# Kernel optimization log

Hardware: AMD Instinct MI355X
Metric: run time of the kernel (lower is better)

Reference implementation:

```python
import jax, jax.numpy as jnp
import numpy as np

DIM = 320
NUM_HEADS = 5
HEAD_DIM = DIM // NUM_HEADS  # 64
SCALE = HEAD_DIM ** -0.5


def setup_inputs() -> dict:
    key = jax.random.key(0)
    k1, k2, k3, k4 = jax.random.split(key, 4)
    B, N, C = 8, 2048, DIM
    x = jax.random.normal(k1, (B, N, C), dtype=jnp.float32)
    # nn.Linear(dim, dim*3, bias=False): weight [3*dim, dim]
    w_qkv = jax.random.normal(k2, (3 * C, C), dtype=jnp.float32) * (C ** -0.5)
    # nn.Linear(dim, dim): weight [dim, dim], bias [dim]
    w_proj = jax.random.normal(k3, (C, C), dtype=jnp.float32) * (C ** -0.5)
    b_proj = jax.random.normal(k4, (C,), dtype=jnp.float32) * 0.01
    return {"x": x, "w_qkv": w_qkv, "w_proj": w_proj, "b_proj": b_proj}


def reference(x, w_qkv, w_proj, b_proj):
    B, N, C = x.shape
    H, D = NUM_HEADS, HEAD_DIM
    # qkv projection: [B, N, 3C] -> [3, B, H, N, D]
    qkv = jnp.einsum('bnc,kc->bnk', x, w_qkv)
    qkv = qkv.reshape(B, N, 3, H, D).transpose(2, 0, 3, 1, 4)
    q, k, v = qkv[0], qkv[1], qkv[2]
    # full attention matrix [B, H, N, N] (retained by original module)
    attn = jnp.einsum('bhnd,bhmd->bhnm', q, k) * SCALE
    attn = jax.nn.softmax(attn, axis=-1)
    # attn_drop p=0 -> identity (eval/deterministic)
    out = jnp.einsum('bhnm,bhmd->bhnd', attn, v)
    out = out.transpose(0, 2, 1, 3).reshape(B, N, C)
    out = jnp.einsum('bnc,oc->bno', out, w_proj) + b_proj
    # proj_drop p=0 -> identity
    return out
```

## Files before the change

### kernel.cpp

```cpp
#include <hip/hip_runtime.h>
#include <hip/hip_bf16.h>


typedef __attribute__((ext_vector_type(8))) short bf16x8;
typedef __attribute__((ext_vector_type(4))) float f32x4;

#define MFMA(a, b, c) __builtin_amdgcn_mfma_f32_16x16x32_bf16((a), (b), (c), 0, 0, 0)

#define QSCALE 0.18033688322643216f

static __device__ inline bf16x8 ld8(const __hip_bfloat16* p) {
    return *reinterpret_cast<const bf16x8*>(p);
}

static __device__ inline unsigned short bfbits(float v) {
    unsigned int u = __builtin_bit_cast(unsigned int, v);
    u += 0x7FFFu + ((u >> 16) & 1u);
    return (unsigned short)(u >> 16);
}

static __device__ inline bf16x8 cvt8(const float* src) {
    float4 a = *reinterpret_cast<const float4*>(src);
    float4 b = *reinterpret_cast<const float4*>(src + 4);
    bf16x8 v;
    v[0] = (short)bfbits(a.x); v[1] = (short)bfbits(a.y);
    v[2] = (short)bfbits(a.z); v[3] = (short)bfbits(a.w);
    v[4] = (short)bfbits(b.x); v[5] = (short)bfbits(b.y);
    v[6] = (short)bfbits(b.z); v[7] = (short)bfbits(b.w);
    return v;
}

__global__ __launch_bounds__(256)
void cvt_x(const float* __restrict__ x, __hip_bfloat16* __restrict__ xb)
{
    const size_t tid = (size_t)blockIdx.x * blockDim.x + threadIdx.x;
    const size_t stride = (size_t)gridDim.x * blockDim.x;
    const float4* x4 = (const float4*)x;
    ushort4* xb4 = (ushort4*)xb;
    for (size_t i = tid; i < 1310720u; i += stride) {
        float4 v = x4[i];
        ushort4 u;
        u.x = bfbits(v.x); u.y = bfbits(v.y);
        u.z = bfbits(v.z); u.w = bfbits(v.w);
        xb4[i] = u;
    }
}

__global__ __launch_bounds__(256)
void qkv_kernel(const __hip_bfloat16* __restrict__ xb,
                const float* __restrict__ w,
                __hip_bfloat16* __restrict__ qout,
                __hip_bfloat16* __restrict__ kp,
                __hip_bfloat16* __restrict__ vp)
{
    __shared__ __align__(16) __hip_bfloat16 As[128 * 72];
    __shared__ __align__(16) __hip_bfloat16 Bs[64 * 72];

    const int tid  = threadIdx.x;
    const int wv   = tid >> 6;
    const int lane = tid & 63;
    const int quad = lane >> 4;
    const int col  = lane & 15;
    const int m0   = blockIdx.x * 128;
    const int n0   = blockIdx.y * 64;

    f32x4 acc[2][4];
#pragma unroll
    for (int i = 0; i < 2; ++i)
#pragma unroll
        for (int j = 0; j < 4; ++j) acc[i][j] = (f32x4){0.f, 0.f, 0.f, 0.f};

    for (int k0 = 0; k0 < 320; k0 += 64) {
        __syncthreads();
#pragma unroll
        for (int i = 0; i < 4; ++i) {
            int ch = tid + i * 256;
            int r = ch >> 3, sg = ch & 7;
            *reinterpret_cast<float4*>(&As[r * 72 + sg * 8]) =
                *reinterpret_cast<const float4*>(&xb[(m0 + r) * 320 + k0 + sg * 8]);
        }
#pragma unroll
        for (int i = 0; i < 2; ++i) {
            int ch = tid + i * 256;
            int r = ch >> 3, sg = ch & 7;
            *reinterpret_cast<bf16x8*>(&Bs[r * 72 + sg * 8]) =
                cvt8(&w[(n0 + r) * 320 + k0 + sg * 8]);
        }
        __syncthreads();

#pragma unroll
        for (int hf = 0; hf < 2; ++hf) {
            bf16x8 a0 = ld8(&As[(wv * 32 + col) * 72 + hf * 32 + quad * 8]);
            bf16x8 a1 = ld8(&As[(wv * 32 + 16 + col) * 72 + hf * 32 + quad * 8]);
#pragma unroll
            for (int nt = 0; nt < 4; ++nt) {
                bf16x8 b = ld8(&Bs[(nt * 16 + col) * 72 + hf * 32 + quad * 8]);
                acc[0][nt] = MFMA(a0, b, acc[0][nt]);
                acc[1][nt] = MFMA(a1, b, acc[1][nt]);
            }
        }
    }

    const int s = blockIdx.y / 5;
    const int h = blockIdx.y % 5;
    unsigned short* qo = (unsigned short*)qout;
    unsigned short* ko = (unsigned short*)kp;
    unsigned short* vo = (unsigned short*)vp;
#pragma unroll
    for (int mt = 0; mt < 2; ++mt) {
#pragma unroll
        for (int nt = 0; nt < 4; ++nt) {
#pragma unroll
            for (int r = 0; r < 4; ++r) {
                int m = m0 + wv * 32 + mt * 16 + quad * 4 + r;
                int d = nt * 16 + col;
                int b = m >> 11, n = m & 2047;
                int bh = b * 5 + h;
                float val = acc[mt][nt][r];
                if (s == 0) {
                    qo[((size_t)bh * 2048 + n) * 64 + d] = bfbits(val * QSCALE);
                } else if (s == 1) {
                    int p = n >> 6, nn = n & 63;
                    size_t a = ((size_t)(bh * 32 + p) * 8 + (d >> 5) * 4 + (nn >> 4)) * 512
                             + (((d >> 3) & 3) * 16 + (nn & 15)) * 8 + (d & 7);
                    ko[a] = bfbits(val);
                } else {
                    int p = n >> 6;
                    size_t a = ((size_t)(bh * 32 + p) * 8 + ((n >> 5) & 1) * 4 + (d >> 4)) * 512
                             + (((n >> 3) & 3) * 16 + (d & 15)) * 8 + (n & 7);
                    vo[a] = bfbits(val);
                }
            }
        }
    }
}

__global__ __launch_bounds__(128)
void attn_kernel(const __hip_bfloat16* __restrict__ Q,
                 const __hip_bfloat16* __restrict__ Kp,
                 const __hip_bfloat16* __restrict__ Vp,
                 __hip_bfloat16* __restrict__ A2)
{
    __shared__ __align__(16) unsigned char smraw[9216];

    const int tid  = threadIdx.x;
    const int wv   = tid >> 6;
    const int lane = tid & 63;
    const int quad = lane >> 4;
    const int col  = lane & 15;
    const int bh = blockIdx.y, b = bh / 5, h = bh % 5;
    const int q0 = blockIdx.x * 32;
    const int t0 = wv * 16;

    __hip_bfloat16* Ps = (__hip_bfloat16*)smraw + wv * 2304;
    unsigned short* ps_w = (unsigned short*)(Ps + (quad * 4) * 72 + col);
    const __hip_bfloat16* ps_r = Ps + col * 72 + quad * 8;

    const __hip_bfloat16* kt = Kp + (size_t)bh * 131072 + (size_t)t0 * 4096 + lane * 8;
    const __hip_bfloat16* vt = Vp + (size_t)bh * 131072 + (size_t)t0 * 4096 + lane * 8;
    const __hip_bfloat16* Qh = Q + (size_t)bh * 131072;

    bf16x8 qf[2][2];
#pragma unroll
    for (int mt = 0; mt < 2; ++mt)
#pragma unroll
        for (int hf = 0; hf < 2; ++hf)
            qf[mt][hf] = ld8(&Qh[(q0 + mt * 16 + col) * 64 + hf * 32 + quad * 8]);

    f32x4 lp[2];
    f32x4 o[2][4];
#pragma unroll
    for (int mt = 0; mt < 2; ++mt) {
        lp[mt] = (f32x4){0.f, 0.f, 0.f, 0.f};
#pragma unroll
        for (int dt = 0; dt < 4; ++dt) o[mt][dt] = (f32x4){0.f, 0.f, 0.f, 0.f};
    }

    bf16x8 ka[8];
#pragma unroll
    for (int f = 0; f < 8; ++f) ka[f] = ld8(kt + f * 512);
    kt += 4096;

    for (int t = 0; t < 16; ++t) {
        f32x4 s[2][4];
#pragma unroll
        for (int mt = 0; mt < 2; ++mt)
#pragma unroll
            for (int nt = 0; nt < 4; ++nt) {
                f32x4 z = (f32x4){0.f, 0.f, 0.f, 0.f};
                z = MFMA(qf[mt][0], ka[nt], z);
                z = MFMA(qf[mt][1], ka[4 + nt], z);
                s[mt][nt] = z;
            }

        bf16x8 va[8];
#pragma unroll
        for (int f = 0; f < 8; ++f) va[f] = ld8(vt + f * 512);
        vt += 4096;

#pragma unroll
        for (int f = 0; f < 8; ++f) ka[f] = ld8(kt + f * 512);
        kt += 4096;

#pragma unroll
        for (int mt = 0; mt < 2; ++mt)
#pragma unroll
            for (int nt = 0; nt < 4; ++nt) {
                f32x4 pv;
#pragma unroll
                for (int r = 0; r < 4; ++r)
                    pv[r] = __builtin_amdgcn_exp2f(s[mt][nt][r]);
                lp[mt] += pv;
#pragma unroll
                for (int r = 0; r < 4; ++r)
                    ps_w[(mt * 16 + r) * 72 + nt * 16] = bfbits(pv[r]);
            }
        __asm__ volatile("s_waitcnt lgkmcnt(0)" ::: "memory");

#pragma unroll
        for (int mt = 0; mt < 2; ++mt)
#pragma unroll
            for (int kk = 0; kk < 2; ++kk) {
                bf16x8 pf = ld8(ps_r + mt * 1152 + kk * 32);
#pragma unroll
                for (int dt = 0; dt < 4; ++dt)
                    o[mt][dt] = MFMA(pf, va[kk * 4 + dt], o[mt][dt]);
            }
    }

    float lval[2][4];
#pragma unroll
    for (int mt = 0; mt < 2; ++mt)
#pragma unroll
        for (int r = 0; r < 4; ++r) {
            float v = lp[mt][r];
#pragma unroll
            for (int off = 1; off < 16; off <<= 1)
                v += __shfl_xor(v, off, 64);
            lval[mt][r] = v;
        }

    float* cbo = (float*)smraw;
    float* cbl = cbo + 2048;
    __syncthreads();
    if (wv == 1) {
#pragma unroll
        for (int mt = 0; mt < 2; ++mt)
#pragma unroll
            for (int dt = 0; dt < 4; ++dt)
#pragma unroll
                for (int r = 0; r < 4; ++r)
                    cbo[(mt * 16 + quad * 4 + r) * 64 + dt * 16 + col] = o[mt][dt][r];
        if (col == 0)
#pragma unroll
            for (int mt = 0; mt < 2; ++mt)
#pragma unroll
                for (int r = 0; r < 4; ++r)
                    cbl[mt * 16 + quad * 4 + r] = lval[mt][r];
    }
    __syncthreads();
    if (wv == 0) {
        unsigned short* a2o = (unsigned short*)A2;
#pragma unroll
        for (int mt = 0; mt < 2; ++mt) {
#pragma unroll
            for (int r = 0; r < 4; ++r) {
                int row = mt * 16 + quad * 4 + r;
                float inv = 1.0f / (lval[mt][r] + cbl[row]);
                int grow = q0 + row;
#pragma unroll
                for (int dt = 0; dt < 4; ++dt) {
                    int d = dt * 16 + col;
                    float val = (o[mt][dt][r] + cbo[row * 64 + d]) * inv;
                    a2o[((size_t)(b * 2048 + grow)) * 320 + h * 64 + d] = bfbits(val);
                }
            }
        }
    }
}

__global__ __launch_bounds__(256)
void proj_kernel(const __hip_bfloat16* __restrict__ a2,
                 const float* __restrict__ w,
                 const float* __restrict__ bias,
                 float* __restrict__ out)
{
    __shared__ __align__(16) __hip_bfloat16 As[128 * 72];
    __shared__ __align__(16) __hip_bfloat16 Bs[64 * 72];

    const int tid  = threadIdx.x;
    const int wv   = tid >> 6;
    const int lane = tid & 63;
    const int quad = lane >> 4;
    const int col  = lane & 15;
    const int m0   = blockIdx.x * 128;
    const int n0   = blockIdx.y * 64;

    f32x4 acc[2][4];
#pragma unroll
    for (int i = 0; i < 2; ++i)
#pragma unroll
        for (int j = 0; j < 4; ++j) acc[i][j] = (f32x4){0.f, 0.f, 0.f, 0.f};

    for (int k0 = 0; k0 < 320; k0 += 64) {
        __syncthreads();
#pragma unroll
        for (int i = 0; i < 4; ++i) {
            int ch = tid + i * 256;
            int r = ch >> 3, sg = ch & 7;
            *reinterpret_cast<float4*>(&As[r * 72 + sg * 8]) =
                *reinterpret_cast<const float4*>(&a2[(m0 + r) * 320 + k0 + sg * 8]);
        }
#pragma unroll
        for (int i = 0; i < 2; ++i) {
            int ch = tid + i * 256;
            int r = ch >> 3, sg = ch & 7;
            *reinterpret_cast<bf16x8*>(&Bs[r * 72 + sg * 8]) =
                cvt8(&w[(n0 + r) * 320 + k0 + sg * 8]);
        }
        __syncthreads();

#pragma unroll
        for (int hf = 0; hf < 2; ++hf) {
            bf16x8 a0 = ld8(&As[(wv * 32 + col) * 72 + hf * 32 + quad * 8]);
            bf16x8 a1 = ld8(&As[(wv * 32 + 16 + col) * 72 + hf * 32 + quad * 8]);
#pragma unroll
            for (int nt = 0; nt < 4; ++nt) {
                bf16x8 b = ld8(&Bs[(nt * 16 + col) * 72 + hf * 32 + quad * 8]);
                acc[0][nt] = MFMA(a0, b, acc[0][nt]);
                acc[1][nt] = MFMA(a1, b, acc[1][nt]);
            }
        }
    }

#pragma unroll
    for (int nt = 0; nt < 4; ++nt) {
        float bv = bias[n0 + nt * 16 + col];
#pragma unroll
        for (int mt = 0; mt < 2; ++mt) {
#pragma unroll
            for (int r = 0; r < 4; ++r) {
                int m = m0 + wv * 32 + mt * 16 + quad * 4 + r;
                out[(size_t)m * 320 + n0 + nt * 16 + col] = acc[mt][nt][r] + bv;
            }
        }
    }
}

extern "C" void kernel_launch(void* const* d_in, const int* in_sizes, int n_in,
                              void* d_out, int out_size, void* d_ws, size_t ws_size,
                              hipStream_t stream)
{
    const float* x      = (const float*)d_in[0];
    const float* w_qkv  = (const float*)d_in[1];
    const float* w_proj = (const float*)d_in[2];
    const float* b_proj = (const float*)d_in[3];
    float* out = (float*)d_out;

    const size_t NX = 5242880;
    __hip_bfloat16* xb = (__hip_bfloat16*)d_ws;
    __hip_bfloat16* q  = xb + NX;
    __hip_bfloat16* kp = q + NX;
    __hip_bfloat16* vp = kp + NX;
    __hip_bfloat16* a2 = xb;

    cvt_x<<<1024, 256, 0, stream>>>(x, xb);
    qkv_kernel<<<dim3(128, 15), 256, 0, stream>>>(xb, w_qkv, q, kp, vp);
    attn_kernel<<<dim3(64, 40), 128, 0, stream>>>(q, kp, vp, a2);
    proj_kernel<<<dim3(128, 5), 256, 0, stream>>>(a2, w_proj, b_proj, out);
}
```

Measured before the change: 187.5 us.

## Compute transposed scores so P feeds PV MFMA from registers, skipping LDS

The QK^T MFMA operands are swapped so each lane holds the score tile transposed. The exponentiated probabilities can then be packed directly into a bf16x4 B operand for the 16x16x16 MFMA, which removes the per-tile LDS write/read round trip and its wait. V is stored in a new 4-element-granular packed layout to match. The epilogue, row-sum reduction and final combine are adjusted for the transposed output accumulator. In exchange it uses twice as many smaller MFMAs and narrower 8-byte V loads.

```diff
diff --git a/kernel.cpp b/kernel.cpp
--- a/kernel.cpp
+++ b/kernel.cpp
@@ -3,9 +3,11 @@
 
 
 typedef __attribute__((ext_vector_type(8))) short bf16x8;
+typedef __attribute__((ext_vector_type(4))) short bf16x4;
 typedef __attribute__((ext_vector_type(4))) float f32x4;
 
-#define MFMA(a, b, c) __builtin_amdgcn_mfma_f32_16x16x32_bf16((a), (b), (c), 0, 0, 0)
+#define MFMA(a, b, c)   __builtin_amdgcn_mfma_f32_16x16x32_bf16((a), (b), (c), 0, 0, 0)
+#define MFMA16(a, b, c) __builtin_amdgcn_mfma_f32_16x16x16bf16_1k((a), (b), (c), 0, 0, 0)
 
 #define QSCALE 0.18033688322643216f
 
@@ -125,9 +127,9 @@
                              + (((d >> 3) & 3) * 16 + (nn & 15)) * 8 + (d & 7);
                     ko[a] = bfbits(val);
                 } else {
-                    int p = n >> 6;
-                    size_t a = ((size_t)(bh * 32 + p) * 8 + ((n >> 5) & 1) * 4 + (d >> 4)) * 512
-                             + (((n >> 3) & 3) * 16 + (d & 15)) * 8 + (n & 7);
+                    int p = n >> 6, n6 = n & 63;
+                    size_t a = ((size_t)(bh * 32 + p) * 16 + (n6 >> 4) * 4 + (d >> 4)) * 256
+                             + (((n6 >> 2) & 3) * 16 + (d & 15)) * 4 + (n6 & 3);
                     vo[a] = bfbits(val);
                 }
             }
@@ -141,7 +143,7 @@
                  const __hip_bfloat16* __restrict__ Vp,
                  __hip_bfloat16* __restrict__ A2)
 {
-    __shared__ __align__(16) unsigned char smraw[9216];
+    __shared__ __align__(16) unsigned char smraw[8448];
 
     const int tid  = threadIdx.x;
     const int wv   = tid >> 6;
@@ -152,12 +154,8 @@
     const int q0 = blockIdx.x * 32;
     const int t0 = wv * 16;
 
-    __hip_bfloat16* Ps = (__hip_bfloat16*)smraw + wv * 2304;
-    unsigned short* ps_w = (unsigned short*)(Ps + (quad * 4) * 72 + col);
-    const __hip_bfloat16* ps_r = Ps + col * 72 + quad * 8;
-
     const __hip_bfloat16* kt = Kp + (size_t)bh * 131072 + (size_t)t0 * 4096 + lane * 8;
-    const __hip_bfloat16* vt = Vp + (size_t)bh * 131072 + (size_t)t0 * 4096 + lane * 8;
+    const __hip_bfloat16* vt = Vp + (size_t)bh * 131072 + (size_t)t0 * 4096 + lane * 4;
     const __hip_bfloat16* Qh = Q + (size_t)bh * 131072;
 
     bf16x8 qf[2][2];
@@ -167,14 +165,14 @@
         for (int hf = 0; hf < 2; ++hf)
             qf[mt][hf] = ld8(&Qh[(q0 + mt * 16 + col) * 64 + hf * 32 + quad * 8]);
 
-    f32x4 lp[2];
-    f32x4 o[2][4];
-#pragma unroll
-    for (int mt = 0; mt < 2; ++mt) {
-        lp[mt] = (f32x4){0.f, 0.f, 0.f, 0.f};
-#pragma unroll
-        for (int dt = 0; dt < 4; ++dt) o[mt][dt] = (f32x4){0.f, 0.f, 0.f, 0.f};
-    }
+    f32x4 lpv[2];
+    f32x4 o[4][2];
+#pragma unroll
+    for (int mt = 0; mt < 2; ++mt) lpv[mt] = (f32x4){0.f, 0.f, 0.f, 0.f};
+#pragma unroll
+    for (int dt = 0; dt < 4; ++dt)
+#pragma unroll
+        for (int mt = 0; mt < 2; ++mt) o[dt][mt] = (f32x4){0.f, 0.f, 0.f, 0.f};
 
     bf16x8 ka[8];
 #pragma unroll
@@ -182,20 +180,21 @@
     kt += 4096;
 
     for (int t = 0; t < 16; ++t) {
-        f32x4 s[2][4];
-#pragma unroll
-        for (int mt = 0; mt < 2; ++mt)
-#pragma unroll
-            for (int nt = 0; nt < 4; ++nt) {
+        f32x4 s[4][2];
+#pragma unroll
+        for (int nt = 0; nt < 4; ++nt)
+#pragma unroll
+            for (int mt = 0; mt < 2; ++mt) {
                 f32x4 z = (f32x4){0.f, 0.f, 0.f, 0.f};
-                z = MFMA(qf[mt][0], ka[nt], z);
-                z = MFMA(qf[mt][1], ka[4 + nt], z);
-                s[mt][nt] = z;
-            }
-
-        bf16x8 va[8];
-#pragma unroll
-        for (int f = 0; f < 8; ++f) va[f] = ld8(vt + f * 512);
+                z = MFMA(ka[nt], qf[mt][0], z);
+                z = MFMA(ka[4 + nt], qf[mt][1], z);
+                s[nt][mt] = z;
+            }
+
+        bf16x4 va[16];
+#pragma unroll
+        for (int f = 0; f < 16; ++f)
+            va[f] = *reinterpret_cast<const bf16x4*>(vt + f * 256);
         vt += 4096;
 
 #pragma unroll
@@ -203,78 +202,63 @@
         kt += 4096;
 
 #pragma unroll
-        for (int mt = 0; mt < 2; ++mt)
-#pragma unroll
-            for (int nt = 0; nt < 4; ++nt) {
+        for (int nt = 0; nt < 4; ++nt) {
+#pragma unroll
+            for (int mt = 0; mt < 2; ++mt) {
                 f32x4 pv;
 #pragma unroll
                 for (int r = 0; r < 4; ++r)
-                    pv[r] = __builtin_amdgcn_exp2f(s[mt][nt][r]);
-                lp[mt] += pv;
-#pragma unroll
-                for (int r = 0; r < 4; ++r)
-                    ps_w[(mt * 16 + r) * 72 + nt * 16] = bfbits(pv[r]);
-            }
-        __asm__ volatile("s_waitcnt lgkmcnt(0)" ::: "memory");
-
-#pragma unroll
-        for (int mt = 0; mt < 2; ++mt)
-#pragma unroll
-            for (int kk = 0; kk < 2; ++kk) {
-                bf16x8 pf = ld8(ps_r + mt * 1152 + kk * 32);
+                    pv[r] = __builtin_amdgcn_exp2f(s[nt][mt][r]);
+                lpv[mt] += pv;
+                bf16x4 pb;
+#pragma unroll
+                for (int r = 0; r < 4; ++r) pb[r] = (short)bfbits(pv[r]);
 #pragma unroll
                 for (int dt = 0; dt < 4; ++dt)
-                    o[mt][dt] = MFMA(pf, va[kk * 4 + dt], o[mt][dt]);
-            }
-    }
-
-    float lval[2][4];
-#pragma unroll
-    for (int mt = 0; mt < 2; ++mt)
-#pragma unroll
-        for (int r = 0; r < 4; ++r) {
-            float v = lp[mt][r];
-#pragma unroll
-            for (int off = 1; off < 16; off <<= 1)
-                v += __shfl_xor(v, off, 64);
-            lval[mt][r] = v;
-        }
+                    o[dt][mt] = MFMA16(va[nt * 4 + dt], pb, o[dt][mt]);
+            }
+        }
+    }
+
+    float lsum[2];
+#pragma unroll
+    for (int mt = 0; mt < 2; ++mt) {
+        float v = lpv[mt][0] + lpv[mt][1] + lpv[mt][2] + lpv[mt][3];
+        v += __shfl_xor(v, 16, 64);
+        v += __shfl_xor(v, 32, 64);
+        lsum[mt] = v;
+    }
 
     float* cbo = (float*)smraw;
     float* cbl = cbo + 2048;
     __syncthreads();
     if (wv == 1) {
 #pragma unroll
-        for (int mt = 0; mt < 2; ++mt)
-#pragma unroll
-            for (int dt = 0; dt < 4; ++dt)
+        for (int dt = 0; dt < 4; ++dt)
+#pragma unroll
+            for (int mt = 0; mt < 2; ++mt)
 #pragma unroll
                 for (int r = 0; r < 4; ++r)
-                    cbo[(mt * 16 + quad * 4 + r) * 64 + dt * 16 + col] = o[mt][dt][r];
-        if (col == 0)
-#pragma unroll
-            for (int mt = 0; mt < 2; ++mt)
-#pragma unroll
-                for (int r = 0; r < 4; ++r)
-                    cbl[mt * 16 + quad * 4 + r] = lval[mt][r];
+                    cbo[(dt * 16 + quad * 4 + r) * 32 + mt * 16 + col] = o[dt][mt][r];
+        if (quad == 0)
+#pragma unroll
+            for (int mt = 0; mt < 2; ++mt) cbl[mt * 16 + col] = lsum[mt];
     }
     __syncthreads();
     if (wv == 0) {
         unsigned short* a2o = (unsigned short*)A2;
 #pragma unroll
         for (int mt = 0; mt < 2; ++mt) {
-#pragma unroll
-            for (int r = 0; r < 4; ++r) {
-                int row = mt * 16 + quad * 4 + r;
-                float inv = 1.0f / (lval[mt][r] + cbl[row]);
-                int grow = q0 + row;
-#pragma unroll
-                for (int dt = 0; dt < 4; ++dt) {
-                    int d = dt * 16 + col;
-                    float val = (o[mt][dt][r] + cbo[row * 64 + d]) * inv;
-                    a2o[((size_t)(b * 2048 + grow)) * 320 + h * 64 + d] = bfbits(val);
+            float inv = 1.0f / (lsum[mt] + cbl[mt * 16 + col]);
+            size_t rowbase = ((size_t)(b * 2048 + q0 + mt * 16 + col)) * 320 + h * 64;
+#pragma unroll
+            for (int dt = 0; dt < 4; ++dt)
+#pragma unroll
+                for (int r = 0; r < 4; ++r) {
+                    int d = dt * 16 + quad * 4 + r;
+                    float val = (o[dt][mt][r] + cbo[d * 32 + mt * 16 + col]) * inv;
+                    a2o[rowbase + d] = bfbits(val);
                 }
-            }
         }
     }
 }
```

New measurement: 190.1 us. No clear change (+1.4%).

## Pre-convert weights to bf16 and compute Q,K,V per head in one block

Applied to the files above, without the earlier changes.

Weight conversion to bf16 moves into the existing x-conversion kernel, so the GEMM kernels load bf16 weights directly instead of converting fp32 on every tile load. The QKV GEMM now has each block compute the Q, K and V outputs for one head, reusing the shared x tile across all three. This cuts the grid from 15 to 5 column blocks and reduces redundant x reads. The cost is 3x the accumulator registers (96 floats) and a larger shared memory footprint, which may reduce occupancy. The grid also shrinks to 640 blocks, which may underfill the GPU.

```diff
diff --git a/kernel.cpp b/kernel.cpp
--- a/kernel.cpp
+++ b/kernel.cpp
@@ -19,24 +19,20 @@
     return (unsigned short)(u >> 16);
 }
 
-static __device__ inline bf16x8 cvt8(const float* src) {
-    float4 a = *reinterpret_cast<const float4*>(src);
-    float4 b = *reinterpret_cast<const float4*>(src + 4);
-    bf16x8 v;
-    v[0] = (short)bfbits(a.x); v[1] = (short)bfbits(a.y);
-    v[2] = (short)bfbits(a.z); v[3] = (short)bfbits(a.w);
-    v[4] = (short)bfbits(b.x); v[5] = (short)bfbits(b.y);
-    v[6] = (short)bfbits(b.z); v[7] = (short)bfbits(b.w);
-    return v;
-}
-
 __global__ __launch_bounds__(256)
-void cvt_x(const float* __restrict__ x, __hip_bfloat16* __restrict__ xb)
+void cvt_all(const float* __restrict__ x, const float* __restrict__ wq,
+             const float* __restrict__ wp,
+             __hip_bfloat16* __restrict__ xb, __hip_bfloat16* __restrict__ wqb,
+             __hip_bfloat16* __restrict__ wpb)
 {
     const size_t tid = (size_t)blockIdx.x * blockDim.x + threadIdx.x;
     const size_t stride = (size_t)gridDim.x * blockDim.x;
     const float4* x4 = (const float4*)x;
+    const float4* wq4 = (const float4*)wq;
+    const float4* wp4 = (const float4*)wp;
     ushort4* xb4 = (ushort4*)xb;
+    ushort4* wqb4 = (ushort4*)wqb;
+    ushort4* wpb4 = (ushort4*)wpb;
     for (size_t i = tid; i < 1310720u; i += stride) {
         float4 v = x4[i];
         ushort4 u;
@@ -44,17 +40,31 @@
         u.z = bfbits(v.z); u.w = bfbits(v.w);
         xb4[i] = u;
     }
+    for (size_t i = tid; i < 76800u; i += stride) {
+        float4 v = wq4[i];
+        ushort4 u;
+        u.x = bfbits(v.x); u.y = bfbits(v.y);
+        u.z = bfbits(v.z); u.w = bfbits(v.w);
+        wqb4[i] = u;
+    }
+    for (size_t i = tid; i < 25600u; i += stride) {
+        float4 v = wp4[i];
+        ushort4 u;
+        u.x = bfbits(v.x); u.y = bfbits(v.y);
+        u.z = bfbits(v.z); u.w = bfbits(v.w);
+        wpb4[i] = u;
+    }
 }
 
 __global__ __launch_bounds__(256)
 void qkv_kernel(const __hip_bfloat16* __restrict__ xb,
-                const float* __restrict__ w,
+                const __hip_bfloat16* __restrict__ wqb,
                 __hip_bfloat16* __restrict__ qout,
                 __hip_bfloat16* __restrict__ kp,
                 __hip_bfloat16* __restrict__ vp)
 {
     __shared__ __align__(16) __hip_bfloat16 As[128 * 72];
-    __shared__ __align__(16) __hip_bfloat16 Bs[64 * 72];
+    __shared__ __align__(16) __hip_bfloat16 Bs[3][64 * 72];
 
     const int tid  = threadIdx.x;
     const int wv   = tid >> 6;
@@ -62,13 +72,15 @@
     const int quad = lane >> 4;
     const int col  = lane & 15;
     const int m0   = blockIdx.x * 128;
-    const int n0   = blockIdx.y * 64;
-
-    f32x4 acc[2][4];
-#pragma unroll
-    for (int i = 0; i < 2; ++i)
-#pragma unroll
-        for (int j = 0; j < 4; ++j) acc[i][j] = (f32x4){0.f, 0.f, 0.f, 0.f};
+    const int h    = blockIdx.y;
+
+    f32x4 acc[3][2][4];
+#pragma unroll
+    for (int s = 0; s < 3; ++s)
+#pragma unroll
+        for (int i = 0; i < 2; ++i)
+#pragma unroll
+            for (int j = 0; j < 4; ++j) acc[s][i][j] = (f32x4){0.f, 0.f, 0.f, 0.f};
 
     for (int k0 = 0; k0 < 320; k0 += 64) {
         __syncthreads();
@@ -80,12 +92,15 @@
                 *reinterpret_cast<const float4*>(&xb[(m0 + r) * 320 + k0 + sg * 8]);
         }
 #pragma unroll
-        for (int i = 0; i < 2; ++i) {
-            int ch = tid + i * 256;
-            int r = ch >> 3, sg = ch & 7;
-            *reinterpret_cast<bf16x8*>(&Bs[r * 72 + sg * 8]) =
-                cvt8(&w[(n0 + r) * 320 + k0 + sg * 8]);
-        }
+        for (int s = 0; s < 3; ++s)
+#pragma unroll
+            for (int i = 0; i < 2; ++i) {
+                int ch = tid + i * 256;
+                int r = ch >> 3, sg = ch & 7;
+                *reinterpret_cast<float4*>(&Bs[s][r * 72 + sg * 8]) =
+                    *reinterpret_cast<const float4*>(
+                        &wqb[((s * 5 + h) * 64 + r) * 320 + k0 + sg * 8]);
+            }
         __syncthreads();
 
 #pragma unroll
@@ -93,42 +108,45 @@
             bf16x8 a0 = ld8(&As[(wv * 32 + col) * 72 + hf * 32 + quad * 8]);
             bf16x8 a1 = ld8(&As[(wv * 32 + 16 + col) * 72 + hf * 32 + quad * 8]);
 #pragma unroll
-            for (int nt = 0; nt < 4; ++nt) {
-                bf16x8 b = ld8(&Bs[(nt * 16 + col) * 72 + hf * 32 + quad * 8]);
-                acc[0][nt] = MFMA(a0, b, acc[0][nt]);
-                acc[1][nt] = MFMA(a1, b, acc[1][nt]);
-            }
-        }
-    }
-
-    const int s = blockIdx.y / 5;
-    const int h = blockIdx.y % 5;
+            for (int s = 0; s < 3; ++s)
+#pragma unroll
+                for (int nt = 0; nt < 4; ++nt) {
+                    bf16x8 b = ld8(&Bs[s][(nt * 16 + col) * 72 + hf * 32 + quad * 8]);
+                    acc[s][0][nt] = MFMA(a0, b, acc[s][0][nt]);
+                    acc[s][1][nt] = MFMA(a1, b, acc[s][1][nt]);
+                }
+        }
+    }
+
     unsigned short* qo = (unsigned short*)qout;
     unsigned short* ko = (unsigned short*)kp;
     unsigned short* vo = (unsigned short*)vp;
 #pragma unroll
-    for (int mt = 0; mt < 2; ++mt) {
-#pragma unroll
-        for (int nt = 0; nt < 4; ++nt) {
-#pragma unroll
-            for (int r = 0; r < 4; ++r) {
-                int m = m0 + wv * 32 + mt * 16 + quad * 4 + r;
-                int d = nt * 16 + col;
-                int b = m >> 11, n = m & 2047;
-                int bh = b * 5 + h;
-                float val = acc[mt][nt][r];
-                if (s == 0) {
-                    qo[((size_t)bh * 2048 + n) * 64 + d] = bfbits(val * QSCALE);
-                } else if (s == 1) {
-                    int p = n >> 6, nn = n & 63;
-                    size_t a = ((size_t)(bh * 32 + p) * 8 + (d >> 5) * 4 + (nn >> 4)) * 512
-                             + (((d >> 3) & 3) * 16 + (nn & 15)) * 8 + (d & 7);
-                    ko[a] = bfbits(val);
-                } else {
-                    int p = n >> 6;
-                    size_t a = ((size_t)(bh * 32 + p) * 8 + ((n >> 5) & 1) * 4 + (d >> 4)) * 512
-                             + (((n >> 3) & 3) * 16 + (d & 15)) * 8 + (n & 7);
-                    vo[a] = bfbits(val);
+    for (int s = 0; s < 3; ++s) {
+#pragma unroll
+        for (int mt = 0; mt < 2; ++mt) {
+#pragma unroll
+            for (int nt = 0; nt < 4; ++nt) {
+#pragma unroll
+                for (int r = 0; r < 4; ++r) {
+                    int m = m0 + wv * 32 + mt * 16 + quad * 4 + r;
+                    int d = nt * 16 + col;
+                    int b = m >> 11, n = m & 2047;
+                    int bh = b * 5 + h;
+                    float val = acc[s][mt][nt][r];
+                    if (s == 0) {
+                        qo[((size_t)bh * 2048 + n) * 64 + d] = bfbits(val * QSCALE);
+                    } else if (s == 1) {
+                        int p = n >> 6, nn = n & 63;
+                        size_t a = ((size_t)(bh * 32 + p) * 8 + (d >> 5) * 4 + (nn >> 4)) * 512
+                                 + (((d >> 3) & 3) * 16 + (nn & 15)) * 8 + (d & 7);
+                        ko[a] = bfbits(val);
+                    } else {
+                        int p = n >> 6;
+                        size_t a = ((size_t)(bh * 32 + p) * 8 + ((n >> 5) & 1) * 4 + (d >> 4)) * 512
+                                 + (((n >> 3) & 3) * 16 + (d & 15)) * 8 + (n & 7);
+                        vo[a] = bfbits(val);
+                    }
                 }
             }
         }
@@ -281,7 +299,7 @@
 
 __global__ __launch_bounds__(256)
 void proj_kernel(const __hip_bfloat16* __restrict__ a2,
-                 const float* __restrict__ w,
+                 const __hip_bfloat16* __restrict__ wpb,
                  const float* __restrict__ bias,
                  float* __restrict__ out)
 {
@@ -315,8 +333,8 @@
         for (int i = 0; i < 2; ++i) {
             int ch = tid + i * 256;
             int r = ch >> 3, sg = ch & 7;
-            *reinterpret_cast<bf16x8*>(&Bs[r * 72 + sg * 8]) =
-                cvt8(&w[(n0 + r) * 320 + k0 + sg * 8]);
+            *reinterpret_cast<float4*>(&Bs[r * 72 + sg * 8]) =
+                *reinterpret_cast<const float4*>(&wpb[(n0 + r) * 320 + k0 + sg * 8]);
         }
         __syncthreads();
 
@@ -357,15 +375,17 @@
     const float* b_proj = (const float*)d_in[3];
     float* out = (float*)d_out;
 
-    const size_t NX = 5242880;
-    __hip_bfloat16* xb = (__hip_bfloat16*)d_ws;
-    __hip_bfloat16* q  = xb + NX;
-    __hip_bfloat16* kp = q + NX;
-    __hip_bfloat16* vp = kp + NX;
-    __hip_bfloat16* a2 = xb;
-
-    cvt_x<<<1024, 256, 0, stream>>>(x, xb);
-    qkv_kernel<<<dim3(128, 15), 256, 0, stream>>>(xb, w_qkv, q, kp, vp);
+    const size_t NX = 5242880, NWQ = 307200, NWP = 102400;
+    __hip_bfloat16* xb  = (__hip_bfloat16*)d_ws;
+    __hip_bfloat16* wqb = xb + NX;
+    __hip_bfloat16* wpb = wqb + NWQ;
+    __hip_bfloat16* q   = wpb + NWP;
+    __hip_bfloat16* kp  = q + NX;
+    __hip_bfloat16* vp  = kp + NX;
+    __hip_bfloat16* a2  = xb;
+
+    cvt_all<<<1024, 256, 0, stream>>>(x, w_qkv, w_proj, xb, wqb, wpb);
+    qkv_kernel<<<dim3(128, 5), 256, 0, stream>>>(xb, wqb, q, kp, vp);
     attn_kernel<<<dim3(64, 40), 128, 0, stream>>>(q, kp, vp, a2);
-    proj_kernel<<<dim3(128, 5), 256, 0, stream>>>(a2, w_proj, b_proj, out);
-}
+    proj_kernel<<<dim3(128, 5), 256, 0, stream>>>(a2, wpb, b_proj, out);
+}
```

Measured after the change: 207.1 us. +10.4%, slower.
